# Kernel optimization log

Measured on AMD Instinct MI355X. Metric: run time of the kernel, lower is better.

Reference implementation:

```python
import jax, jax.numpy as jnp
import numpy as np

NUM_CLASSES = 80
FOCAL_ALPHA = 0.25
FOCAL_GAMMA = 2.0
HUBER_SIGMA = 3.0
REG_MEAN = 0.0
REG_STD = 0.2
POS_THRESH = 0.5
NEG_THRESH = 0.4
EPS = 1e-4


def _iou(anchors, boxes):
    # anchors [A,4], boxes [M,4] -> [A,M]
    a = anchors[:, None, :]
    b = boxes[None, :, :]
    iw = jnp.clip(jnp.minimum(a[..., 2], b[..., 2]) - jnp.maximum(a[..., 0], b[..., 0]), 0.0)
    ih = jnp.clip(jnp.minimum(a[..., 3], b[..., 3]) - jnp.maximum(a[..., 1], b[..., 1]), 0.0)
    inter = iw * ih
    area_a = (a[..., 2] - a[..., 0]) * (a[..., 3] - a[..., 1])
    area_b = (b[..., 2] - b[..., 0]) * (b[..., 3] - b[..., 1])
    return inter / jnp.clip(area_a + area_b - inter, 1e-8)


def _bbox_transform(anchors, gt):
    # keras-retinanet style: per-coordinate offsets normalized by anchor w/h
    aw = anchors[:, 2] - anchors[:, 0]
    ah = anchors[:, 3] - anchors[:, 1]
    t = jnp.stack([(gt[:, 0] - anchors[:, 0]) / aw,
                   (gt[:, 1] - anchors[:, 1]) / ah,
                   (gt[:, 2] - anchors[:, 2]) / aw,
                   (gt[:, 3] - anchors[:, 3]) / ah], axis=1)
    return (t - REG_MEAN) / REG_STD


def _targets_one_image(anchor, ann, image_shape):
    # anchor [A,4], ann [M,5]
    iou = _iou(anchor, ann[:, :4])              # [A,M]
    best = jnp.argmax(iou, axis=1)              # [A]
    max_iou = jnp.max(iou, axis=1)
    pos = max_iou >= POS_THRESH
    ign = (max_iou > NEG_THRESH) & (~pos)
    states = jnp.where(pos, 1.0, jnp.where(ign, -1.0, 0.0))
    # ignore anchors whose center falls outside the image
    cx = (anchor[:, 0] + anchor[:, 2]) * 0.5
    cy = (anchor[:, 1] + anchor[:, 3]) * 0.5
    outside = (cx >= image_shape[1].astype(cx.dtype)) | (cy >= image_shape[0].astype(cy.dtype))
    states = jnp.where(outside, -1.0, states)
    assigned = ann[best]                        # [A,5]
    labels = jax.nn.one_hot(assigned[:, 4].astype(jnp.int32), NUM_CLASSES, dtype=anchor.dtype)
    labels = labels * pos[:, None].astype(anchor.dtype)
    regression = _bbox_transform(anchor, assigned[:, :4])
    return regression, labels, states


def setup_inputs() -> dict:
    key = jax.random.key(0)
    B, A, C, M = 8, 120000, NUM_CLASSES, 32
    k = jax.random.split(key, 10)
    # anchors: random centers/sizes inside an 800x800 image
    cx = jax.random.uniform(k[0], (B, A), minval=0.0, maxval=800.0)
    cy = jax.random.uniform(k[1], (B, A), minval=0.0, maxval=800.0)
    w = jax.random.uniform(k[2], (B, A), minval=16.0, maxval=256.0)
    h = jax.random.uniform(k[3], (B, A), minval=16.0, maxval=256.0)
    anchors = jnp.stack([cx - w / 2, cy - h / 2, cx + w / 2, cy + h / 2], axis=-1)
    # annotations: valid boxes (x1<x2, y1<y2) + class id
    x1 = jax.random.uniform(k[4], (B, M), minval=0.0, maxval=600.0)
    y1 = jax.random.uniform(k[5], (B, M), minval=0.0, maxval=600.0)
    bw = jax.random.uniform(k[6], (B, M), minval=32.0, maxval=180.0)
    bh = jax.random.uniform(k[7], (B, M), minval=32.0, maxval=180.0)
    cls = jax.random.randint(k[8], (B, M), 0, C).astype(jnp.float32)
    batch_annotations = jnp.stack([x1, y1, x1 + bw, y1 + bh, cls], axis=-1)
    # make sure positives exist: first M anchors per image ~= GT boxes (small jitter)
    jitter = 2.0 * jax.random.normal(k[9], (B, M, 4))
    anchors = anchors.at[:, :M, :].set(batch_annotations[:, :, :4] + jitter)
    output_classification = jax.random.uniform(jax.random.fold_in(key, 1), (B, A, C), minval=0.01, maxval=0.99)
    output_regression = jax.random.normal(jax.random.fold_in(key, 2), (B, A, 4))
    image_shape = jnp.array([800, 800], dtype=jnp.int32)
    return {"output_regression": output_regression,
            "output_classification": output_classification,
            "batch_annotations": batch_annotations,
            "anchors": anchors,
            "image_shape": image_shape}


def reference(output_regression, output_classification, batch_annotations, anchors, image_shape):
    reg_t, lab_t, states = jax.vmap(lambda a, an: _targets_one_image(a, an, image_shape))(
        anchors, batch_annotations)
    num_pos = jnp.sum((states == 1.0).astype(jnp.float32))
    normalizer = jnp.maximum(num_pos, 1.0)
    # focal loss (classification output already sigmoid probabilities)
    valid = (states != -1.0)[..., None].astype(output_classification.dtype)
    p = jnp.clip(output_classification, EPS, 1.0 - EPS)
    is_pos = lab_t == 1.0
    alpha_factor = jnp.where(is_pos, FOCAL_ALPHA, 1.0 - FOCAL_ALPHA)
    focal_weight = alpha_factor * jnp.where(is_pos, 1.0 - p, p) ** FOCAL_GAMMA
    bce = -(lab_t * jnp.log(p) + (1.0 - lab_t) * jnp.log1p(-p))
    cls_loss = jnp.sum(focal_weight * bce * valid) / normalizer
    # smooth L1 on positive anchors
    sigma_sq = HUBER_SIGMA ** 2
    diff = jnp.abs(output_regression - reg_t)
    sl1 = jnp.where(diff < 1.0 / sigma_sq, 0.5 * sigma_sq * diff * diff, diff - 0.5 / sigma_sq)
    pos_mask = (states == 1.0)[..., None].astype(output_regression.dtype)
    reg_loss = jnp.sum(sl1 * pos_mask) / normalizer
    return cls_loss + reg_loss
```

## Files before the change

### kernel.cpp

```cpp
#include <hip/hip_runtime.h>
#include <hip/hip_bf16.h>


#define CLS 80
#define F4_PER_ANCHOR (CLS / 4)
#define MAXM 32
#define APB 256

__global__ void __launch_bounds__(256)
fused_kernel(const float* __restrict__ anchors,
             const float* __restrict__ ann,
             const float* __restrict__ out_reg,
             const float* __restrict__ cls,
             const int*   __restrict__ image_shape,
             float* __restrict__ part,
             int A) {
    __shared__ float s_ann[MAXM * 5];
    __shared__ float s_area[MAXM];
    __shared__ int   s_meta[APB];
    __shared__ float s_red[4][3];

    const int b   = blockIdx.y;
    const int tid = threadIdx.x;
    const int a0  = blockIdx.x * APB;

    const float* annb = ann + (size_t)b * MAXM * 5;
    if (tid < MAXM * 5) s_ann[tid] = annb[tid];
    __syncthreads();
    if (tid < MAXM) {
        const float x1 = s_ann[tid*5+0], y1 = s_ann[tid*5+1];
        const float x2 = s_ann[tid*5+2], y2 = s_ann[tid*5+3];
        s_area[tid] = (x2 - x1) * (y2 - y1);
    }
    __syncthreads();

    float regv = 0.0f, cntv = 0.0f;
    const int a = a0 + tid;
    if (a < A) {
        const size_t idx = (size_t)b * A + a;
        const float4 an = ((const float4*)anchors)[idx];
        const float area_a = (an.z - an.x) * (an.w - an.y);

        float inter_b = 0.0f, union_b = 1.0f;
        int best = 0;
        #pragma unroll
        for (int j = 0; j < MAXM; ++j) {
            const float bx1 = s_ann[j*5+0], by1 = s_ann[j*5+1];
            const float bx2 = s_ann[j*5+2], by2 = s_ann[j*5+3];
            const float iw = fmaxf(fminf(an.z, bx2) - fmaxf(an.x, bx1), 0.0f);
            const float ih = fmaxf(fminf(an.w, by2) - fmaxf(an.y, by1), 0.0f);
            const float inter = iw * ih;
            const float uni = fmaxf(area_a + s_area[j] - inter, 1e-8f);
            if (inter * union_b > inter_b * uni) {
                inter_b = inter; union_b = uni; best = j;
            }
        }

        const bool pos = (2.0f * inter_b >= union_b);
        const bool ign = (inter_b > 0.4f * union_b) && !pos;
        const float cx = (an.x + an.z) * 0.5f;
        const float cy = (an.y + an.w) * 0.5f;
        const bool outside = (cx >= (float)image_shape[1]) || (cy >= (float)image_shape[0]);

        int state = pos ? 1 : (ign ? -1 : 0);
        if (outside) state = -1;

        s_meta[tid] = (state == -1) ? -2
                    : (state == 1) ? (int)s_ann[best*5+4]
                                   : -1;

        if (state == 1) {
            const float aw = an.z - an.x;
            const float ah = an.w - an.y;
            const float t0 = ((s_ann[best*5+0] - an.x) / aw) * 5.0f;
            const float t1 = ((s_ann[best*5+1] - an.y) / ah) * 5.0f;
            const float t2 = ((s_ann[best*5+2] - an.z) / aw) * 5.0f;
            const float t3 = ((s_ann[best*5+3] - an.w) / ah) * 5.0f;
            const float4 r = ((const float4*)out_reg)[idx];
            const float d0 = fabsf(r.x - t0), d1 = fabsf(r.y - t1);
            const float d2 = fabsf(r.z - t2), d3 = fabsf(r.w - t3);
            float reg = 0.0f;
            reg += (d0 < (1.0f/9.0f)) ? (4.5f*d0*d0) : (d0 - (0.5f/9.0f));
            reg += (d1 < (1.0f/9.0f)) ? (4.5f*d1*d1) : (d1 - (0.5f/9.0f));
            reg += (d2 < (1.0f/9.0f)) ? (4.5f*d2*d2) : (d2 - (0.5f/9.0f));
            reg += (d3 < (1.0f/9.0f)) ? (4.5f*d3*d3) : (d3 - (0.5f/9.0f));
            regv = reg;
            cntv = 1.0f;
        }
    } else {
        s_meta[tid] = -2;
    }
    __syncthreads();

    const float4* cls4 = (const float4*)cls
                       + ((size_t)b * A + a0) * F4_PER_ANCHOR;
    float clsv = 0.0f;
    const int nA = min(APB, A - a0);

    if (nA == APB) {
        #pragma unroll 5
        for (int it = 0; it < F4_PER_ANCHOR; ++it) {
            const int i  = tid + it * APB;
            const int al = i / F4_PER_ANCHOR;
            const float4 p4 = cls4[i];
            const int lab = s_meta[al];
            const float valid = (lab == -2) ? 0.0f : 1.0f;
            const int c0 = (i - al * F4_PER_ANCHOR) * 4;

            const float pv[4] = {p4.x, p4.y, p4.z, p4.w};
            #pragma unroll
            for (int k = 0; k < 4; ++k) {
                const float p  = fminf(fmaxf(pv[k], 1e-4f), 1.0f - 1e-4f);
                const bool is_pos = (lab == c0 + k);
                const float pt    = is_pos ? (1.0f - p) : p;
                const float scale = (is_pos ? 0.25f : 0.75f) * valid;
                clsv += scale * pt * pt * (-__logf(1.0f - pt));
            }
        }
    } else {
        const int nf4 = nA * F4_PER_ANCHOR;
        for (int i = tid; i < nf4; i += APB) {
            const int al = i / F4_PER_ANCHOR;
            const float4 p4 = cls4[i];
            const int lab = s_meta[al];
            const float valid = (lab == -2) ? 0.0f : 1.0f;
            const int c0 = (i - al * F4_PER_ANCHOR) * 4;

            const float pv[4] = {p4.x, p4.y, p4.z, p4.w};
            #pragma unroll
            for (int k = 0; k < 4; ++k) {
                const float p  = fminf(fmaxf(pv[k], 1e-4f), 1.0f - 1e-4f);
                const bool is_pos = (lab == c0 + k);
                const float pt    = is_pos ? (1.0f - p) : p;
                const float scale = (is_pos ? 0.25f : 0.75f) * valid;
                clsv += scale * pt * pt * (-__logf(1.0f - pt));
            }
        }
    }

    #pragma unroll
    for (int off = 32; off > 0; off >>= 1) {
        clsv += __shfl_down(clsv, off, 64);
        regv += __shfl_down(regv, off, 64);
        cntv += __shfl_down(cntv, off, 64);
    }
    const int lane = tid & 63, wid = tid >> 6;
    if (lane == 0) { s_red[wid][0] = clsv; s_red[wid][1] = regv; s_red[wid][2] = cntv; }
    __syncthreads();
    if (tid == 0) {
        const int blk = blockIdx.y * gridDim.x + blockIdx.x;
        part[blk*3+0] = s_red[0][0] + s_red[1][0] + s_red[2][0] + s_red[3][0];
        part[blk*3+1] = s_red[0][1] + s_red[1][1] + s_red[2][1] + s_red[3][1];
        part[blk*3+2] = s_red[0][2] + s_red[1][2] + s_red[2][2] + s_red[3][2];
    }
}

__global__ void final_kernel(const float* __restrict__ part, int n_blk,
                             float* __restrict__ out) {
    float cl = 0.0f, r = 0.0f, c = 0.0f;
    for (int i = threadIdx.x; i < n_blk; i += blockDim.x) {
        cl += part[i*3+0];
        r  += part[i*3+1];
        c  += part[i*3+2];
    }
    #pragma unroll
    for (int off = 32; off > 0; off >>= 1) {
        cl += __shfl_down(cl, off, 64);
        r  += __shfl_down(r,  off, 64);
        c  += __shfl_down(c,  off, 64);
    }
    __shared__ float red[16][3];
    const int lane = threadIdx.x & 63, wid = threadIdx.x >> 6;
    if (lane == 0) { red[wid][0] = cl; red[wid][1] = r; red[wid][2] = c; }
    __syncthreads();
    if (threadIdx.x == 0) {
        float cls = 0.0f, rs = 0.0f, cs = 0.0f;
        const int nw = blockDim.x >> 6;
        for (int w = 0; w < nw; ++w) { cls += red[w][0]; rs += red[w][1]; cs += red[w][2]; }
        out[0] = (cls + rs) / fmaxf(cs, 1.0f);
    }
}

extern "C" void kernel_launch(void* const* d_in, const int* in_sizes, int n_in,
                              void* d_out, int out_size, void* d_ws, size_t ws_size,
                              hipStream_t stream) {
    const float* out_reg = (const float*)d_in[0];
    const float* out_cls = (const float*)d_in[1];
    const float* ann     = (const float*)d_in[2];
    const float* anchors = (const float*)d_in[3];
    const int*   ishape  = (const int*)d_in[4];
    float* out = (float*)d_out;

    const int B  = in_sizes[2] / (MAXM * 5);
    const int BA = in_sizes[0] / 4;
    const int A  = BA / B;

    float* part = (float*)d_ws;

    const int gx = (A + APB - 1) / APB;
    dim3 g1(gx, B);
    fused_kernel<<<g1, APB, 0, stream>>>(anchors, ann, out_reg, out_cls,
                                         ishape, part, A);

    final_kernel<<<1, 1024, 0, stream>>>(part, gx * B, out);
}
```

Before: 441.8 us.

## Prefetch classification tiles before IoU matching and double-buffer loads

The anchor load and the first batch of five classification float4 loads are issued before the IoU matching loop, so memory latency overlaps the matching compute. The classification loop is restructured into four groups of five loads, double-buffered in registers with non-temporal hints. One shared-memory sync is removed by computing annotation areas directly from global memory. This adds register pressure (ten live float4 buffers), which could lower occupancy.

```diff
diff --git a/kernel.cpp b/kernel.cpp
--- a/kernel.cpp
+++ b/kernel.cpp
@@ -6,6 +6,8 @@
 #define F4_PER_ANCHOR (CLS / 4)
 #define MAXM 32
 #define APB 256
+
+typedef float f32x4 __attribute__((ext_vector_type(4)));
 
 __global__ void __launch_bounds__(256)
 fused_kernel(const float* __restrict__ anchors,
@@ -23,23 +25,35 @@
     const int b   = blockIdx.y;
     const int tid = threadIdx.x;
     const int a0  = blockIdx.x * APB;
+    const int a   = a0 + tid;
+    const int nA  = min(APB, A - a0);
+    const bool full = (nA == APB);
+
+    const size_t idx = (size_t)b * A + a;
+
+    f32x4 an = {0.0f, 0.0f, 0.0f, 0.0f};
+    if (a < A) an = ((const f32x4*)anchors)[idx];
 
     const float* annb = ann + (size_t)b * MAXM * 5;
     if (tid < MAXM * 5) s_ann[tid] = annb[tid];
-    __syncthreads();
     if (tid < MAXM) {
-        const float x1 = s_ann[tid*5+0], y1 = s_ann[tid*5+1];
-        const float x2 = s_ann[tid*5+2], y2 = s_ann[tid*5+3];
+        const float x1 = annb[tid*5+0], y1 = annb[tid*5+1];
+        const float x2 = annb[tid*5+2], y2 = annb[tid*5+3];
         s_area[tid] = (x2 - x1) * (y2 - y1);
     }
     __syncthreads();
 
+    const f32x4* cls4 = (const f32x4*)cls + ((size_t)b * A + a0) * F4_PER_ANCHOR;
+    f32x4 pipe[2][5];
+    if (full) {
+        #pragma unroll
+        for (int u = 0; u < 5; ++u)
+            pipe[0][u] = __builtin_nontemporal_load(cls4 + tid + u * APB);
+    }
+
     float regv = 0.0f, cntv = 0.0f;
-    const int a = a0 + tid;
     if (a < A) {
-        const size_t idx = (size_t)b * A + a;
-        const float4 an = ((const float4*)anchors)[idx];
-        const float area_a = (an.z - an.x) * (an.w - an.y);
+        const float area_a = (an[2] - an[0]) * (an[3] - an[1]);
 
         float inter_b = 0.0f, union_b = 1.0f;
         int best = 0;
@@ -47,8 +61,8 @@
         for (int j = 0; j < MAXM; ++j) {
             const float bx1 = s_ann[j*5+0], by1 = s_ann[j*5+1];
             const float bx2 = s_ann[j*5+2], by2 = s_ann[j*5+3];
-            const float iw = fmaxf(fminf(an.z, bx2) - fmaxf(an.x, bx1), 0.0f);
-            const float ih = fmaxf(fminf(an.w, by2) - fmaxf(an.y, by1), 0.0f);
+            const float iw = fmaxf(fminf(an[2], bx2) - fmaxf(an[0], bx1), 0.0f);
+            const float ih = fmaxf(fminf(an[3], by2) - fmaxf(an[1], by1), 0.0f);
             const float inter = iw * ih;
             const float uni = fmaxf(area_a + s_area[j] - inter, 1e-8f);
             if (inter * union_b > inter_b * uni) {
@@ -58,8 +72,8 @@
 
         const bool pos = (2.0f * inter_b >= union_b);
         const bool ign = (inter_b > 0.4f * union_b) && !pos;
-        const float cx = (an.x + an.z) * 0.5f;
-        const float cy = (an.y + an.w) * 0.5f;
+        const float cx = (an[0] + an[2]) * 0.5f;
+        const float cy = (an[1] + an[3]) * 0.5f;
         const bool outside = (cx >= (float)image_shape[1]) || (cy >= (float)image_shape[0]);
 
         int state = pos ? 1 : (ign ? -1 : 0);
@@ -70,15 +84,15 @@
                                    : -1;
 
         if (state == 1) {
-            const float aw = an.z - an.x;
-            const float ah = an.w - an.y;
-            const float t0 = ((s_ann[best*5+0] - an.x) / aw) * 5.0f;
-            const float t1 = ((s_ann[best*5+1] - an.y) / ah) * 5.0f;
-            const float t2 = ((s_ann[best*5+2] - an.z) / aw) * 5.0f;
-            const float t3 = ((s_ann[best*5+3] - an.w) / ah) * 5.0f;
-            const float4 r = ((const float4*)out_reg)[idx];
-            const float d0 = fabsf(r.x - t0), d1 = fabsf(r.y - t1);
-            const float d2 = fabsf(r.z - t2), d3 = fabsf(r.w - t3);
+            const float aw = an[2] - an[0];
+            const float ah = an[3] - an[1];
+            const float t0 = ((s_ann[best*5+0] - an[0]) / aw) * 5.0f;
+            const float t1 = ((s_ann[best*5+1] - an[1]) / ah) * 5.0f;
+            const float t2 = ((s_ann[best*5+2] - an[2]) / aw) * 5.0f;
+            const float t3 = ((s_ann[best*5+3] - an[3]) / ah) * 5.0f;
+            const f32x4 r = ((const f32x4*)out_reg)[idx];
+            const float d0 = fabsf(r[0] - t0), d1 = fabsf(r[1] - t1);
+            const float d2 = fabsf(r[2] - t2), d3 = fabsf(r[3] - t3);
             float reg = 0.0f;
             reg += (d0 < (1.0f/9.0f)) ? (4.5f*d0*d0) : (d0 - (0.5f/9.0f));
             reg += (d1 < (1.0f/9.0f)) ? (4.5f*d1*d1) : (d1 - (0.5f/9.0f));
@@ -92,49 +106,41 @@
     }
     __syncthreads();
 
-    const float4* cls4 = (const float4*)cls
-                       + ((size_t)b * A + a0) * F4_PER_ANCHOR;
     float clsv = 0.0f;
-    const int nA = min(APB, A - a0);
-
-    if (nA == APB) {
-        #pragma unroll 5
-        for (int it = 0; it < F4_PER_ANCHOR; ++it) {
-            const int i  = tid + it * APB;
-            const int al = i / F4_PER_ANCHOR;
-            const float4 p4 = cls4[i];
-            const int lab = s_meta[al];
-            const float valid = (lab == -2) ? 0.0f : 1.0f;
-            const int c0 = (i - al * F4_PER_ANCHOR) * 4;
-
-            const float pv[4] = {p4.x, p4.y, p4.z, p4.w};
+
+    auto focal4 = [&](const f32x4 v, const int i) {
+        const int al  = (int)((unsigned)i / 20u);
+        const int lab = s_meta[al];
+        const float valid = (lab == -2) ? 0.0f : 1.0f;
+        const int c0 = (i - al * F4_PER_ANCHOR) * 4;
+        #pragma unroll
+        for (int k = 0; k < 4; ++k) {
+            const float p  = fminf(fmaxf(v[k], 1e-4f), 1.0f - 1e-4f);
+            const bool is_pos = (lab == c0 + k);
+            const float pt    = is_pos ? (1.0f - p) : p;
+            const float scale = (is_pos ? 0.25f : 0.75f) * valid;
+            clsv += scale * pt * pt * (-__logf(1.0f - pt));
+        }
+    };
+
+    if (full) {
+        #pragma unroll
+        for (int g = 0; g < 4; ++g) {
+            if (g < 3) {
+                #pragma unroll
+                for (int u = 0; u < 5; ++u)
+                    pipe[(g + 1) & 1][u] =
+                        __builtin_nontemporal_load(cls4 + tid + ((g + 1) * 5 + u) * APB);
+            }
             #pragma unroll
-            for (int k = 0; k < 4; ++k) {
-                const float p  = fminf(fmaxf(pv[k], 1e-4f), 1.0f - 1e-4f);
-                const bool is_pos = (lab == c0 + k);
-                const float pt    = is_pos ? (1.0f - p) : p;
-                const float scale = (is_pos ? 0.25f : 0.75f) * valid;
-                clsv += scale * pt * pt * (-__logf(1.0f - pt));
-            }
+            for (int u = 0; u < 5; ++u)
+                focal4(pipe[g & 1][u], tid + (g * 5 + u) * APB);
         }
     } else {
         const int nf4 = nA * F4_PER_ANCHOR;
         for (int i = tid; i < nf4; i += APB) {
-            const int al = i / F4_PER_ANCHOR;
-            const float4 p4 = cls4[i];
-            const int lab = s_meta[al];
-            const float valid = (lab == -2) ? 0.0f : 1.0f;
-            const int c0 = (i - al * F4_PER_ANCHOR) * 4;
-
-            const float pv[4] = {p4.x, p4.y, p4.z, p4.w};
-            #pragma unroll
-            for (int k = 0; k < 4; ++k) {
-                const float p  = fminf(fmaxf(pv[k], 1e-4f), 1.0f - 1e-4f);
-                const bool is_pos = (lab == c0 + k);
-                const float pt    = is_pos ? (1.0f - p) : p;
-                const float scale = (is_pos ? 0.25f : 0.75f) * valid;
-                clsv += scale * pt * pt * (-__logf(1.0f - pt));
-            }
+            const f32x4 v = __builtin_nontemporal_load(cls4 + i);
+            focal4(v, i);
         }
     }
 
```

New measurement: 437.3 us. About the same (-1.0%).
